# Performance work log

Measured on AMD Instinct MI355X. Metric: run time of the kernel, lower is better.

The kernel has to match this reference:

```python
import jax, jax.numpy as jnp
import numpy as np
from jax import lax

EMBED_DIM = 64

def _dwconv(x, w, b):
    # x: [B,H,W,C], w: [3,3,1,C] (HWIO depthwise), b: [C]
    c = x.shape[-1]
    y = lax.conv_general_dilated(
        x, w, window_strides=(1, 1), padding='SAME',
        dimension_numbers=('NHWC', 'HWIO', 'NHWC'),
        feature_group_count=c)
    return y + b

def setup_inputs() -> dict:
    key = jax.random.key(0)
    ks = jax.random.split(key, 8)
    B, H, W, C = 8, 56, 56, 64
    x = jax.random.normal(ks[0], (B, H, W, C), dtype=jnp.float32)
    wq = jax.random.normal(ks[1], (3, 3, 1, C), dtype=jnp.float32) * 0.1
    wk = jax.random.normal(ks[2], (3, 3, 1, C), dtype=jnp.float32) * 0.1
    wv = jax.random.normal(ks[3], (3, 3, 1, C), dtype=jnp.float32) * 0.1
    bq = jnp.zeros((C,), jnp.float32)
    bk = jnp.zeros((C,), jnp.float32)
    bv = jnp.zeros((C,), jnp.float32)
    Wp = jax.random.normal(ks[4], (C, EMBED_DIM), dtype=jnp.float32) * (1.0 / np.sqrt(C))
    bp = jnp.zeros((EMBED_DIM,), jnp.float32)
    return {"x": x, "wq": wq, "bq": bq, "wk": wk, "bk": bk,
            "wv": wv, "bv": bv, "Wp": Wp, "bp": bp}

def reference(x, wq, bq, wk, bk, wv, bv, Wp, bp):
    B, H, W, C = x.shape
    scale = EMBED_DIM ** (-0.5)  # original DIVIDES by this (i.e. multiplies by sqrt(d))
    q = _dwconv(x, wq, bq).reshape(B, H * W, C)
    k = _dwconv(x, wk, bk).reshape(B, H * W, C)
    v = _dwconv(x, wv, bv).reshape(B, H * W, C)
    scores = jnp.einsum('bnc,bmc->bnm', q, k) / scale  # [B, N, N]
    att = jax.nn.softmax(scores, axis=-1)
    ctx = jnp.einsum('bnm,bmc->bnc', att, v).reshape(B, H, W, C)
    return ctx @ Wp + bp
```

## Files before the change

### kernel.cpp

```cpp
#include <hip/hip_runtime.h>
#include <math.h>
#include <stdint.h>

#define B_ 8
#define H_ 56
#define W_ 56
#define C_ 64
#define N_ (H_*W_)
#define KT 32
#define NCH (N_/KT)
#define KSPLIT 8
#define SCALE_LOG2 11.5415603271f

typedef float    f32x16 __attribute__((ext_vector_type(16)));
typedef short    short8 __attribute__((ext_vector_type(8)));
typedef unsigned u32x4  __attribute__((ext_vector_type(4)));

static __device__ __forceinline__ float bf16lo_f(unsigned w) { return __uint_as_float(w << 16); }
static __device__ __forceinline__ float bf16hi_f(unsigned w) { return __uint_as_float(w & 0xFFFF0000u); }
static __device__ __forceinline__ unsigned pack_bf2(float a, float b) {
    unsigned r;
    asm("v_cvt_pk_bf16_f32 %0, %1, %2" : "=v"(r) : "v"(a), "v"(b));
    return r;
}
static __device__ __forceinline__ float exp2_fast(float x) {
    float r;
    asm("v_exp_f32 %0, %1" : "=v"(r) : "v"(x));
    return r;
}
static __device__ __forceinline__ short8 frag_words(unsigned w0, unsigned w1, unsigned w2, unsigned w3) {
    union { u32x4 u; short8 s; } t;
    t.u = (u32x4){w0, w1, w2, w3};
    return t.s;
}
static __device__ __forceinline__ f32x16 MF(short8 a, short8 b, f32x16 c) {
    return __builtin_amdgcn_mfma_f32_32x32x16_bf16(a, b, c, 0, 0, 0);
}
static __device__ __forceinline__ short8 ldf(const uint8_t* p) {
    union { uint4 a; short8 s; } t;
    t.a = *(const uint4*)p;
    return t.s;
}

__global__ __launch_bounds__(256)
void dwconv_fused(const float* __restrict__ x,
                  const float* __restrict__ wq, const float* __restrict__ bq,
                  const float* __restrict__ wk, const float* __restrict__ bk,
                  const float* __restrict__ wv, const float* __restrict__ bv,
                  uint8_t* __restrict__ qf, uint8_t* __restrict__ kf,
                  uint8_t* __restrict__ vf) {
    __shared__ float tq[32][68];
    __shared__ float tk[32][68];

    const int t   = threadIdx.x;
    const int c   = t & 63;
    const int oct = t >> 6;
    const int og  = blockIdx.x * 4 + oct;
    const int b   = og / (N_ / 8);
    const int po  = og % (N_ / 8);
    const int h0  = po / 7;
    const int w0  = (po - h0 * 7) * 8;

    float q8[8], k8[8], v8[8];
    const float bqc = bq[c], bkc = bk[c], bvc = bv[c];
    #pragma unroll
    for (int i = 0; i < 8; ++i) { q8[i] = bqc; k8[i] = bkc; v8[i] = bvc; }

    #pragma unroll
    for (int dh = 0; dh < 3; ++dh) {
        int hh = h0 + dh - 1;
        if (hh < 0 || hh >= H_) continue;
        float xv[10];
        #pragma unroll
        for (int j = 0; j < 10; ++j) {
            int ww = w0 + j - 1;
            xv[j] = (ww >= 0 && ww < W_) ? x[(((size_t)b * H_ + hh) * W_ + ww) * C_ + c] : 0.f;
        }
        #pragma unroll
        for (int dw = 0; dw < 3; ++dw) {
            float fq = wq[(dh * 3 + dw) * C_ + c];
            float fk = wk[(dh * 3 + dw) * C_ + c];
            float fv = wv[(dh * 3 + dw) * C_ + c];
            #pragma unroll
            for (int i = 0; i < 8; ++i) {
                float xs = xv[i + dw];
                q8[i] = fmaf(xs, fq, q8[i]);
                k8[i] = fmaf(xs, fk, k8[i]);
                v8[i] = fmaf(xs, fv, v8[i]);
            }
        }
    }
    #pragma unroll
    for (int i = 0; i < 8; ++i) q8[i] *= SCALE_LOG2;

    {
        uint4 vh4; unsigned* vh = (unsigned*)&vh4;
        #pragma unroll
        for (int j = 0; j < 4; ++j) vh[j] = pack_bf2(v8[2*j], v8[2*j+1]);
        *(uint4*)&vf[((size_t)(og >> 2)) * 4096 + (og & 3) * 1024 + c * 16] = vh4;
    }

    #pragma unroll
    for (int i = 0; i < 8; ++i) { tq[oct * 8 + i][c] = q8[i]; tk[oct * 8 + i][c] = k8[i]; }
    __syncthreads();

    const int g2 = t & 7;
    const int tl = t >> 3;
    float qv[8], kv[8];
    *(float4*)&qv[0] = *(const float4*)&tq[tl][8 * g2];
    *(float4*)&qv[4] = *(const float4*)&tq[tl][8 * g2 + 4];
    *(float4*)&kv[0] = *(const float4*)&tk[tl][8 * g2];
    *(float4*)&kv[4] = *(const float4*)&tk[tl][8 * g2 + 4];

    uint4 qh4, ql4, kh4, kl4;
    unsigned* qh = (unsigned*)&qh4; unsigned* ql = (unsigned*)&ql4;
    unsigned* kh = (unsigned*)&kh4; unsigned* kl = (unsigned*)&kl4;
    #pragma unroll
    for (int j = 0; j < 4; ++j) {
        float a0 = qv[2*j], a1 = qv[2*j+1];
        qh[j] = pack_bf2(a0, a1);
        ql[j] = pack_bf2(a0 - bf16lo_f(qh[j] & 0xFFFFu), a1 - bf16hi_f(qh[j]));
        float k0 = kv[2*j], k1 = kv[2*j+1];
        kh[j] = pack_bf2(k0, k1);
        kl[j] = pack_bf2(k0 - bf16lo_f(kh[j] & 0xFFFFu), k1 - bf16hi_f(kh[j]));
    }
    const int nf = blockIdx.x * 32 + tl;
    const size_t tb = ((size_t)(nf >> 5)) * 8192;
    *(uint4*)&qf[tb +        g2 * 512 + tl * 16] = qh4;
    *(uint4*)&qf[tb + 4096 + g2 * 512 + tl * 16] = ql4;
    *(uint4*)&kf[tb +        g2 * 512 + tl * 16] = kh4;
    *(uint4*)&kf[tb + 4096 + g2 * 512 + tl * 16] = kl4;
}

__global__ __launch_bounds__(64, 4)
void attn_part(const uint8_t* __restrict__ qf, const uint8_t* __restrict__ kf,
               const uint8_t* __restrict__ vf,
               float* __restrict__ part, float* __restrict__ ml) {
    const int lane = threadIdx.x;
    const int h    = lane >> 5;
    const int l31  = lane & 31;
    const int bx   = blockIdx.x;
    const int b    = bx & 7;
    const int r    = bx >> 3;
    const int ks   = r / NCH;
    const int qt   = r % NCH;

    const int c_beg = (NCH * ks) / KSPLIT;
    const int c_end = (NCH * (ks + 1)) / KSPLIT;

    const uint8_t* qb = qf + ((size_t)(b * NCH + qt)) * 8192;
    short8 qh[4], ql[4];
    #pragma unroll
    for (int s = 0; s < 4; ++s) {
        qh[s] = ldf(qb + s * 1024 + lane * 16);
        ql[s] = ldf(qb + 4096 + s * 1024 + lane * 16);
    }

    f32x16 ctx0, ctx1;
    #pragma unroll
    for (int i = 0; i < 16; ++i) { ctx0[i] = 0.f; ctx1[i] = 0.f; }
    float mrun = -INFINITY, lrun = 0.f;

    for (int ch = c_beg; ch < c_end; ++ch) {
        const uint8_t* kb = kf + ((size_t)(b * NCH + ch)) * 8192;
        const uint8_t* vb = vf + ((size_t)(b * NCH + ch)) * 4096;
        short8 kh0 = ldf(kb +        lane * 16);
        short8 kh1 = ldf(kb + 1024 + lane * 16);
        short8 kh2 = ldf(kb + 2048 + lane * 16);
        short8 kh3 = ldf(kb + 3072 + lane * 16);
        short8 kl0 = ldf(kb + 4096 + lane * 16);
        short8 kl1 = ldf(kb + 5120 + lane * 16);
        short8 kl2 = ldf(kb + 6144 + lane * 16);
        short8 kl3 = ldf(kb + 7168 + lane * 16);
        short8 v00 = ldf(vb +        h * 1024 + l31 * 16);
        short8 v10 = ldf(vb +  512 + h * 1024 + l31 * 16);
        short8 v01 = ldf(vb + 2048 + h * 1024 + l31 * 16);
        short8 v11 = ldf(vb + 2560 + h * 1024 + l31 * 16);

        f32x16 s0;
        #pragma unroll
        for (int i = 0; i < 16; ++i) s0[i] = 0.f;
        s0 = MF(kh0, qh[0], s0); s0 = MF(kh0, ql[0], s0); s0 = MF(kl0, qh[0], s0);
        s0 = MF(kh1, qh[1], s0); s0 = MF(kh1, ql[1], s0); s0 = MF(kl1, qh[1], s0);
        s0 = MF(kh2, qh[2], s0); s0 = MF(kh2, ql[2], s0); s0 = MF(kl2, qh[2], s0);
        s0 = MF(kh3, qh[3], s0); s0 = MF(kh3, ql[3], s0); s0 = MF(kl3, qh[3], s0);

        float t0 = fmaxf(fmaxf(s0[0],  s0[1]),  s0[2]);
        float t1 = fmaxf(fmaxf(s0[3],  s0[4]),  s0[5]);
        float t2 = fmaxf(fmaxf(s0[6],  s0[7]),  s0[8]);
        float t3 = fmaxf(fmaxf(s0[9],  s0[10]), s0[11]);
        float t4 = fmaxf(fmaxf(s0[12], s0[13]), s0[14]);
        float mloc = fmaxf(fmaxf(fmaxf(t0, t1), s0[15]), fmaxf(fmaxf(t2, t3), t4));
        float mw = fmaxf(mloc, __shfl_xor(mloc, 32));
        if (mw > mrun + 8.f) {
            float fac = exp2_fast(mrun - mw);
            lrun *= fac;
            #pragma unroll
            for (int i = 0; i < 16; ++i) { ctx0[i] *= fac; ctx1[i] *= fac; }
            mrun = mw;
        }
        float p0[16];
        float lsum = 0.f;
        #pragma unroll
        for (int i = 0; i < 16; ++i) { p0[i] = exp2_fast(s0[i] - mrun); lsum += p0[i]; }
        lrun += lsum + __shfl_xor(lsum, 32);

        unsigned hw0[8], lw0[8];
        #pragma unroll
        for (int j = 0; j < 8; ++j) {
            hw0[j] = pack_bf2(p0[2*j], p0[2*j+1]);
            lw0[j] = pack_bf2(p0[2*j]   - bf16lo_f(hw0[j] & 0xFFFFu),
                              p0[2*j+1] - bf16hi_f(hw0[j]));
        }

#define PV_STEP(S, VA, VB) {                                                  \
        const int base = 4 * (S);                                             \
        unsigned a0 = hw0[base], a1 = hw0[base+1], a2 = hw0[base+2], a3 = hw0[base+3]; \
        unsigned c0 = lw0[base], c1 = lw0[base+1], c2 = lw0[base+2], c3 = lw0[base+3]; \
        unsigned sh0 = __shfl_xor(h ? a0 : a2, 32);                           \
        unsigned sh1 = __shfl_xor(h ? a1 : a3, 32);                           \
        unsigned sl0 = __shfl_xor(h ? c0 : c2, 32);                           \
        unsigned sl1 = __shfl_xor(h ? c1 : c3, 32);                           \
        short8 bh = frag_words(h ? sh0 : a0, h ? sh1 : a1,                    \
                               h ? a2 : sh0, h ? a3 : sh1);                   \
        short8 bl = frag_words(h ? sl0 : c0, h ? sl1 : c1,                    \
                               h ? c2 : sl0, h ? c3 : sl1);                   \
        ctx0 = MF(VA, bh, ctx0);  ctx1 = MF(VB, bh, ctx1);                    \
        ctx0 = MF(VA, bl, ctx0);  ctx1 = MF(VB, bl, ctx1);                    \
    }
        PV_STEP(0, v00, v10)
        PV_STEP(1, v01, v11)
#undef PV_STEP
    }

    float* pbase = part + (size_t)bx * 2048 + l31;
    #pragma unroll
    for (int u = 0; u < 4; ++u)
        #pragma unroll
        for (int rr = 0; rr < 4; ++rr) {
            int cc = 8 * u + 4 * h + rr;
            pbase[(size_t)cc * 32]        = ctx0[4*u + rr];
            pbase[(size_t)(cc + 32) * 32] = ctx1[4*u + rr];
        }
    if (h == 0)
        ((float2*)ml)[(size_t)bx * 32 + l31] = make_float2(mrun, lrun);
}

__global__ __launch_bounds__(256)
void combine(const float* __restrict__ part, const float* __restrict__ ml,
             const float* __restrict__ Wp, const float* __restrict__ bp,
             float* __restrict__ out) {
    __shared__ float cm[64][68];
    __shared__ float fac[KSPLIT][64];

    const int bx = blockIdx.x;
    const int b  = bx & 7;
    const int g  = bx >> 3;
    const int t  = threadIdx.x;

    if (t < 64) {
        const int qt   = g * 2 + (t >> 5);
        const int qrow = t & 31;
        float m8[KSPLIT], l8[KSPLIT];
        #pragma unroll
        for (int ks = 0; ks < KSPLIT; ++ks) {
            float2 v = ((const float2*)ml)[((size_t)(((ks * NCH + qt) << 3) | b)) * 32 + qrow];
            m8[ks] = v.x; l8[ks] = v.y;
        }
        float M = m8[0];
        #pragma unroll
        for (int ks = 1; ks < KSPLIT; ++ks) M = fmaxf(M, m8[ks]);
        float L = 0.f;
        float f[KSPLIT];
        #pragma unroll
        for (int ks = 0; ks < KSPLIT; ++ks) { f[ks] = exp2f(m8[ks] - M); L = fmaf(l8[ks], f[ks], L); }
        float inv = 1.f / L;
        #pragma unroll
        for (int ks = 0; ks < KSPLIT; ++ks) fac[ks][t] = f[ks] * inv;
    }
    __syncthreads();

    #pragma unroll
    for (int rep = 0; rep < 4; ++rep) {
        const int idx = rep * 256 + t;
        const int c   = idx >> 4;
        const int q   = (idx & 15) * 4;
        const int qt  = g * 2 + (q >> 5);
        const int qr  = q & 31;
        float4 acc = make_float4(0.f, 0.f, 0.f, 0.f);
        #pragma unroll
        for (int ks = 0; ks < KSPLIT; ++ks) {
            const float4 p4 = *(const float4*)&part[((size_t)(((ks * NCH + qt) << 3) | b)) * 2048
                                                    + c * 32 + qr];
            const float4 f4 = *(const float4*)&fac[ks][q];
            acc.x = fmaf(p4.x, f4.x, acc.x);
            acc.y = fmaf(p4.y, f4.y, acc.y);
            acc.z = fmaf(p4.z, f4.z, acc.z);
            acc.w = fmaf(p4.w, f4.w, acc.w);
        }
        *(float4*)&cm[c][q] = acc;
    }
    __syncthreads();

    {
        const int q = t >> 2, eq = t & 3;
        float4 y[4];
        #pragma unroll
        for (int e = 0; e < 4; ++e) y[e] = *(const float4*)&bp[eq * 16 + e * 4];
        for (int cc = 0; cc < 64; ++cc) {
            float v = cm[cc][q];
            const float4* w4 = (const float4*)&Wp[cc * 64 + eq * 16];
            #pragma unroll
            for (int e = 0; e < 4; ++e) {
                float4 wv4 = w4[e];
                y[e].x = fmaf(v, wv4.x, y[e].x);
                y[e].y = fmaf(v, wv4.y, y[e].y);
                y[e].z = fmaf(v, wv4.z, y[e].z);
                y[e].w = fmaf(v, wv4.w, y[e].w);
            }
        }
        const int n = g * 64 + q;
        float4* op = (float4*)&out[((size_t)b * N_ + n) * 64 + eq * 16];
        #pragma unroll
        for (int e = 0; e < 4; ++e) op[e] = y[e];
    }
}

extern "C" void kernel_launch(void* const* d_in, const int* in_sizes, int n_in,
                              void* d_out, int out_size, void* d_ws, size_t ws_size,
                              hipStream_t stream) {
    const float* x  = (const float*)d_in[0];
    const float* wq = (const float*)d_in[1];
    const float* bq = (const float*)d_in[2];
    const float* wk = (const float*)d_in[3];
    const float* bk = (const float*)d_in[4];
    const float* wv = (const float*)d_in[5];
    const float* bv = (const float*)d_in[6];
    const float* Wp = (const float*)d_in[7];
    const float* bp = (const float*)d_in[8];
    float* out = (float*)d_out;

    const size_t qk_bytes = (size_t)B_ * NCH * 8192;
    const size_t vf_bytes = (size_t)B_ * NCH * 4096;
    uint8_t* qf = (uint8_t*)d_ws;
    uint8_t* kf = qf + qk_bytes;
    uint8_t* vf = kf + qk_bytes;
    float*   partp = (float*)(vf + vf_bytes);
    float*   mlp   = partp + (size_t)6272 * 2048;

    dwconv_fused<<<784, 256, 0, stream>>>(x, wq, bq, wk, bk, wv, bv, qf, kf, vf);
    attn_part<<<KSPLIT * NCH * 8, 64, 0, stream>>>(qf, kf, vf, partp, mlp);
    combine<<<49 * 8, 256, 0, stream>>>(partp, mlp, Wp, bp, out);
}
```

Before: 182.9 us.

## Halve key split count and store partial attention outputs as packed bf16

Reduces the key-dimension split from 8 to 4, halving the number of attn_part blocks and partial results to combine. Partial context outputs are stored as packed bf16 pairs (channel c and c+32 in one word) instead of fp32, cutting intermediate write and read traffic, and combine is rewritten to unpack them. This lowers parallelism in attn_part (fewer blocks, longer per-block loops) and adds bf16 rounding error to the partial sums.

```diff
diff --git a/kernel.cpp b/kernel.cpp
--- a/kernel.cpp
+++ b/kernel.cpp
@@ -9,7 +9,7 @@
 #define N_ (H_*W_)
 #define KT 32
 #define NCH (N_/KT)
-#define KSPLIT 8
+#define KSPLIT 4
 #define SCALE_LOG2 11.5415603271f
 
 typedef float    f32x16 __attribute__((ext_vector_type(16)));
@@ -135,7 +135,7 @@
 __global__ __launch_bounds__(64, 4)
 void attn_part(const uint8_t* __restrict__ qf, const uint8_t* __restrict__ kf,
                const uint8_t* __restrict__ vf,
-               float* __restrict__ part, float* __restrict__ ml) {
+               unsigned* __restrict__ part, float* __restrict__ ml) {
     const int lane = threadIdx.x;
     const int h    = lane >> 5;
     const int l31  = lane & 31;
@@ -233,21 +233,21 @@
 #undef PV_STEP
     }
 
-    float* pbase = part + (size_t)bx * 2048 + l31;
+    unsigned* pbase = part + (size_t)bx * 1024;
     #pragma unroll
     for (int u = 0; u < 4; ++u)
         #pragma unroll
         for (int rr = 0; rr < 4; ++rr) {
-            int cc = 8 * u + 4 * h + rr;
-            pbase[(size_t)cc * 32]        = ctx0[4*u + rr];
-            pbase[(size_t)(cc + 32) * 32] = ctx1[4*u + rr];
+            const int i  = 4 * u + rr;
+            const int cc = 8 * u + 4 * h + rr;
+            pbase[cc * 32 + l31] = pack_bf2(ctx0[i], ctx1[i]);
         }
     if (h == 0)
         ((float2*)ml)[(size_t)bx * 32 + l31] = make_float2(mrun, lrun);
 }
 
 __global__ __launch_bounds__(256)
-void combine(const float* __restrict__ part, const float* __restrict__ ml,
+void combine(const unsigned* __restrict__ part, const float* __restrict__ ml,
              const float* __restrict__ Wp, const float* __restrict__ bp,
              float* __restrict__ out) {
     __shared__ float cm[64][68];
@@ -281,24 +281,28 @@
     __syncthreads();
 
     #pragma unroll
-    for (int rep = 0; rep < 4; ++rep) {
-        const int idx = rep * 256 + t;
-        const int c   = idx >> 4;
-        const int q   = (idx & 15) * 4;
-        const int qt  = g * 2 + (q >> 5);
-        const int qr  = q & 31;
-        float4 acc = make_float4(0.f, 0.f, 0.f, 0.f);
+    for (int rep = 0; rep < 2; ++rep) {
+        const int cp = t >> 3;
+        const int q4 = t & 7;
+        float accL[4] = {0.f, 0.f, 0.f, 0.f};
+        float accH[4] = {0.f, 0.f, 0.f, 0.f};
         #pragma unroll
         for (int ks = 0; ks < KSPLIT; ++ks) {
-            const float4 p4 = *(const float4*)&part[((size_t)(((ks * NCH + qt) << 3) | b)) * 2048
-                                                    + c * 32 + qr];
-            const float4 f4 = *(const float4*)&fac[ks][q];
-            acc.x = fmaf(p4.x, f4.x, acc.x);
-            acc.y = fmaf(p4.y, f4.y, acc.y);
-            acc.z = fmaf(p4.z, f4.z, acc.z);
-            acc.w = fmaf(p4.w, f4.w, acc.w);
-        }
-        *(float4*)&cm[c][q] = acc;
+            const uint4 w4 = *(const uint4*)&part[((size_t)(((ks * NCH + g * 2 + rep) << 3) | b)) * 1024
+                                                  + cp * 32 + q4 * 4];
+            const unsigned* w = (const unsigned*)&w4;
+            #pragma unroll
+            for (int j = 0; j < 4; ++j) {
+                const float fj = fac[ks][rep * 32 + q4 * 4 + j];
+                accL[j] = fmaf(bf16lo_f(w[j]), fj, accL[j]);
+                accH[j] = fmaf(bf16hi_f(w[j]), fj, accH[j]);
+            }
+        }
+        #pragma unroll
+        for (int j = 0; j < 4; ++j) {
+            cm[cp][rep * 32 + q4 * 4 + j]      = accL[j];
+            cm[cp + 32][rep * 32 + q4 * 4 + j] = accH[j];
+        }
     }
     __syncthreads();
 
@@ -342,11 +346,11 @@
 
     const size_t qk_bytes = (size_t)B_ * NCH * 8192;
     const size_t vf_bytes = (size_t)B_ * NCH * 4096;
-    uint8_t* qf = (uint8_t*)d_ws;
-    uint8_t* kf = qf + qk_bytes;
-    uint8_t* vf = kf + qk_bytes;
-    float*   partp = (float*)(vf + vf_bytes);
-    float*   mlp   = partp + (size_t)6272 * 2048;
+    uint8_t*  qf = (uint8_t*)d_ws;
+    uint8_t*  kf = qf + qk_bytes;
+    uint8_t*  vf = kf + qk_bytes;
+    unsigned* partp = (unsigned*)(vf + vf_bytes);
+    float*    mlp   = (float*)(partp + (size_t)3136 * 1024);
 
     dwconv_fused<<<784, 256, 0, stream>>>(x, wq, bq, wk, bk, wv, bv, qf, kf, vf);
     attn_part<<<KSPLIT * NCH * 8, 64, 0, stream>>>(qf, kf, vf, partp, mlp);
```

After: 176.3 us. -3.6%, faster.
